# Kernel tuning notes

Measured on AMD Instinct MI355X. Metric: run time of the kernel, lower is better.

Reference implementation:

```python
import jax, jax.numpy as jnp
import numpy as np


def rotary_pos_emb(x):
    # x: [..., seq, dim], dim even. Interleaved (GPT-NeoX-style pairwise) rotary.
    dim, seq = x.shape[-1], x.shape[-2]
    ts = jnp.arange(0, dim, 2, dtype=jnp.float32)
    inv_freqs = 10000.0 ** (-ts / dim)
    grid = jnp.arange(seq, dtype=jnp.float32)[:, None] * inv_freqs[None, :]  # [s, dim//2]
    sin = jnp.repeat(jnp.sin(grid), 2, axis=-1).astype(x.dtype)  # [s, dim]
    cos = jnp.repeat(jnp.cos(grid), 2, axis=-1).astype(x.dtype)  # [s, dim]
    x1, x2 = x[..., ::2], x[..., 1::2]
    xs = jnp.stack([-x2, x1], axis=-1).reshape(x.shape)  # interleave (-x2, x1)
    return x * cos + xs * sin


def setup_inputs() -> dict:
    key = jax.random.key(0)
    kx, kq, kk, kv, ko = jax.random.split(key, 5)
    B, S, D = 2, 2048, 1024
    scale = 1.0 / np.sqrt(D)
    x = jax.random.normal(kx, (B, S, D), dtype=jnp.float32)
    mask = jnp.tril(jnp.ones((S, S), dtype=bool))  # causal
    Wq = jax.random.normal(kq, (D, D), dtype=jnp.float32) * scale
    Wk = jax.random.normal(kk, (D, D), dtype=jnp.float32) * scale
    Wv = jax.random.normal(kv, (D, D), dtype=jnp.float32) * scale
    Wo = jax.random.normal(ko, (D, D), dtype=jnp.float32) * scale
    return {"x": x, "mask": mask, "Wq": Wq, "Wk": Wk, "Wv": Wv, "Wo": Wo}


def reference(x, mask, Wq, Wk, Wv, Wo):
    H = 16
    POS_PORTION = 0.5
    B, S, D = x.shape
    K = D // H
    p = int(K * POS_PORTION)

    q = (x @ Wq) / (K ** 0.5)
    q = q.reshape(B, S, H, K).transpose(0, 2, 1, 3)  # b h l k
    q = jnp.concatenate([rotary_pos_emb(q[..., :p]), q[..., p:]], axis=-1)

    k = (x @ Wk).reshape(B, S, H, K).transpose(0, 2, 1, 3)
    k = jnp.concatenate([rotary_pos_emb(k[..., :p]), k[..., p:]], axis=-1)

    v = (x @ Wv).reshape(B, S, H, K).transpose(0, 2, 1, 3)

    logits = jnp.einsum('bhik,bhjk->bhij', q, k)
    # full-precision masked softmax
    l32 = logits.astype(jnp.float32)
    l32 = jnp.where(mask, l32, -1e30)
    a = jax.nn.softmax(l32, axis=-1).astype(logits.dtype)

    y = jnp.einsum('bhij,bhjv->bhiv', a, v)
    y = y.transpose(0, 2, 1, 3).reshape(B, S, D)  # b l (h v)
    return y @ Wo
```

## Files before the change

### kernel.cpp

```cpp
#include <hip/hip_runtime.h>
#include <cstdint>
#include <cstddef>

typedef __bf16 bf16;
typedef __bf16 bf16x8 __attribute__((ext_vector_type(8)));
typedef float  f32x4  __attribute__((ext_vector_type(4)));
typedef short  s16x4  __attribute__((ext_vector_type(4)));

#define B_  2
#define S_  2048
#define D_  1024
#define H_  16
#define KH  64

__device__ __forceinline__ void gload_lds16(const bf16* gp, bf16* lds_base) {
    __builtin_amdgcn_global_load_lds(
        (const __attribute__((address_space(1))) unsigned int*)gp,
        (__attribute__((address_space(3))) unsigned int*)lds_base,
        16, 0, 0);
}

__global__ __launch_bounds__(256) void prep(
    const float* __restrict__ x, bf16* __restrict__ xb,
    const float* __restrict__ Wq, const float* __restrict__ Wk,
    const float* __restrict__ Wv, const float* __restrict__ Wo,
    bf16* __restrict__ WqkvT, bf16* __restrict__ WoT)
{
    __shared__ bf16 tl[64][72];
    int z = blockIdx.x;
    if (z < 4096) {
        const int i = (z * 256 + threadIdx.x) * 4;
        const float4 v = *(const float4*)(x + i);
        union { int2 w; bf16 e[4]; } u;
        u.e[0] = (bf16)v.x; u.e[1] = (bf16)v.y;
        u.e[2] = (bf16)v.z; u.e[3] = (bf16)v.w;
        *(int2*)(xb + i) = u.w;
        return;
    }
    z -= 4096;
    const int zx = z & 15, zy = (z >> 4) & 15, zw = z >> 8;
    const float* src = (zw == 0) ? Wq : (zw == 1) ? Wk : (zw == 2) ? Wv : Wo;
    bf16* dst = (zw < 3) ? (WqkvT + (size_t)zw * D_ * D_) : WoT;
    const int r0 = zy * 64;
    const int c0 = zx * 64;
    const int t  = threadIdx.x;
    {
        const int r = t >> 2, cs = (t & 3) * 16;
        const float4* p = (const float4*)(src + (size_t)(r0 + r) * D_ + c0 + cs);
        float4 a0 = p[0], a1 = p[1], a2 = p[2], a3 = p[3];
        tl[cs +  0][r] = (bf16)a0.x; tl[cs +  1][r] = (bf16)a0.y;
        tl[cs +  2][r] = (bf16)a0.z; tl[cs +  3][r] = (bf16)a0.w;
        tl[cs +  4][r] = (bf16)a1.x; tl[cs +  5][r] = (bf16)a1.y;
        tl[cs +  6][r] = (bf16)a1.z; tl[cs +  7][r] = (bf16)a1.w;
        tl[cs +  8][r] = (bf16)a2.x; tl[cs +  9][r] = (bf16)a2.y;
        tl[cs + 10][r] = (bf16)a2.z; tl[cs + 11][r] = (bf16)a2.w;
        tl[cs + 12][r] = (bf16)a3.x; tl[cs + 13][r] = (bf16)a3.y;
        tl[cs + 14][r] = (bf16)a3.z; tl[cs + 15][r] = (bf16)a3.w;
    }
    __syncthreads();
    {
        const int c = t >> 2, rs = (t & 3) * 16;
        union { int4 v[2]; bf16 e[16]; } u;
#pragma unroll
        for (int i = 0; i < 16; ++i) u.e[i] = tl[c][rs + i];
        int4* p = (int4*)(dst + (size_t)(c0 + c) * D_ + r0 + rs);
        p[0] = u.v[0]; p[1] = u.v[1];
    }
}

template <int EPI, int BN>
__global__ __launch_bounds__(256, 2) void gemm_bt(
    const bf16* __restrict__ A, const bf16* __restrict__ BT,
    float* __restrict__ C, int N, int Kd,
    bf16* __restrict__ qp, bf16* __restrict__ kp, bf16* __restrict__ vp)
{
    constexpr int NJF = BN / 32;
    __shared__ bf16 As[128 * 64];
    __shared__ bf16 Bs[BN * 64];
    const int tid  = threadIdx.x;
    const int lane = tid & 63;
    const int wave = tid >> 6;
    const int l15  = lane & 15;
    const int quad = lane >> 4;
    const int m0 = blockIdx.y * 128;
    const int n0 = blockIdx.x * BN;
    const int wm = (wave >> 1) * 64;
    const int wn = (wave & 1) * (BN / 2);

    f32x4 acc[4][NJF];
#pragma unroll
    for (int i = 0; i < 4; ++i)
#pragma unroll
        for (int j = 0; j < NJF; ++j) acc[i][j] = f32x4{0.f, 0.f, 0.f, 0.f};

    for (int k0 = 0; k0 < Kd; k0 += 64) {
        __syncthreads();
#pragma unroll
        for (int c = 0; c < 4; ++c) {
            const int base  = wave * 4096 + c * 1024;
            const int flatb = base + lane * 16;
            const int row   = flatb >> 7;
            const int col   = (flatb & 127) >> 1;
            gload_lds16(A + (size_t)(m0 + row) * Kd + k0 + col, As + (base >> 1));
        }
#pragma unroll
        for (int c = 0; c < NJF; ++c) {
            const int base  = wave * (BN * 32) + c * 1024;
            const int flatb = base + lane * 16;
            const int row   = flatb >> 7;
            const int col   = (flatb & 127) >> 1;
            gload_lds16(BT + (size_t)(n0 + row) * Kd + k0 + col, Bs + (base >> 1));
        }
        __syncthreads();
#pragma unroll
        for (int kk = 0; kk < 64; kk += 32) {
            bf16x8 af[4], bfv[NJF];
#pragma unroll
            for (int i = 0; i < 4; ++i)
                af[i] = *(const bf16x8*)&As[(wm + i * 16 + l15) * 64 + kk + quad * 8];
#pragma unroll
            for (int j = 0; j < NJF; ++j)
                bfv[j] = *(const bf16x8*)&Bs[(wn + j * 16 + l15) * 64 + kk + quad * 8];
#pragma unroll
            for (int i = 0; i < 4; ++i)
#pragma unroll
                for (int j = 0; j < NJF; ++j)
                    acc[i][j] = __builtin_amdgcn_mfma_f32_16x16x32_bf16(
                        af[i], bfv[j], acc[i][j], 0, 0, 0);
        }
    }

#pragma unroll
    for (int i = 0; i < 4; ++i)
#pragma unroll
        for (int j = 0; j < NJF; ++j) {
            const int Rb = m0 + wm + i * 16 + quad * 4;
            const int Cc = n0 + wn + j * 16 + l15;
            if (EPI == 0) {
#pragma unroll
                for (int r = 0; r < 4; ++r)
                    C[(size_t)(Rb + r) * N + Cc] = acc[i][j][r];
            } else {
                const int sec = Cc >> 10, cc = Cc & 1023;
                const int h = cc >> 6, kd = cc & 63;
                if (sec == 2) {
                    const int b = Rb >> 11, s0 = Rb & (S_ - 1);
                    union { s16x4 sv; bf16 e[4]; } pv;
#pragma unroll
                    for (int r = 0; r < 4; ++r) pv.e[r] = (bf16)acc[i][j][r];
                    *(s16x4*)&vp[((size_t)(b * H_ + h) * KH + kd) * S_ + s0] = pv.sv;
                } else {
#pragma unroll
                    for (int r = 0; r < 4; ++r) {
                        const int row = Rb + r;
                        const int b = row >> 11, s = row & (S_ - 1);
                        float v = acc[i][j][r];
                        if (sec == 0) {
                            qp[((size_t)(b * H_ + h) * S_ + s) * KH + kd] =
                                (bf16)(v * 0.1803368801111204f);
                        } else {
                            if ((kd >> 4) < 2) {
                                const float partner = __shfl_xor(v, 1);
                                const float inv = __builtin_exp2f(
                                    -(float)(kd >> 1) * (13.28771237954945f / 16.f));
                                const float ang = (float)s * inv;
                                float sn, cn;
                                __sincosf(ang, &sn, &cn);
                                v = (l15 & 1) ? fmaf(partner, sn, v * cn)
                                              : fmaf(-partner, sn, v * cn);
                            }
                            kp[((size_t)(b * H_ + h) * S_ + s) * KH + kd] = (bf16)v;
                        }
                    }
                }
            }
        }
}

__global__ __launch_bounds__(256, 4) void attn(
    const bf16* __restrict__ q, const bf16* __restrict__ k,
    const bf16* __restrict__ vt, bf16* __restrict__ y)
{
    __shared__ bf16 Ks[2][64 * 64];
    __shared__ bf16 VTs[2][64 * 64];

    const int z  = blockIdx.x;
    const int v_ = z & 7;
    const int u_ = (z >> 3) & 31;
    const int w_ = z >> 8;
    const int bh = u_;
    const int qt = (w_ == 0) ? v_ : (w_ == 1) ? (15 - v_)
                 : (w_ == 2) ? (16 + v_) : (31 - v_);
    const int b  = bh >> 4, h = bh & 15;
    const int t    = threadIdx.x;
    const int lane = t & 63, wave = t >> 6;
    const int l15  = lane & 15, quad = lane >> 4;
    const int wrow = qt * 64 + wave * 16;

    const bf16* kbh = k  + (size_t)bh * S_ * KH;
    const bf16* vbh = vt + (size_t)bh * KH * S_;

    const int srow = lane >> 3;
    const int sg   = (lane & 7) ^ srow;

    auto stage = [&](int jt, int bb) {
        const int j0 = jt * 64;
#pragma unroll
        for (int i = 0; i < 2; ++i) {
            const int c = wave * 2 + i;
            gload_lds16(kbh + (size_t)(j0 + c * 8 + srow) * KH + sg * 8,
                        &Ks[bb][c * 8 * 64]);
            gload_lds16(vbh + (size_t)(c * 8 + srow) * S_ + j0 + sg * 8,
                        &VTs[bb][c * 8 * 64]);
        }
    };

    bf16x8 qf[2];
    {
        const bf16* qp = q + ((size_t)bh * S_ + wrow + l15) * KH + quad * 8;
        qf[0] = *(const bf16x8*)qp;
        qf[1] = *(const bf16x8*)(qp + 32);
        const float s = (float)(wrow + l15);
#pragma unroll
        for (int tt = 0; tt < 4; ++tt) {
            const int i = quad * 4 + tt;
            const float inv = exp2f(-(float)i * (13.28771237954945f / 16.f));
            const float ang = s * inv;
            const float sn = sinf(ang), cn = cosf(ang);
            const float x0 = (float)qf[0][2 * tt], x1 = (float)qf[0][2 * tt + 1];
            qf[0][2 * tt]     = (bf16)(x0 * cn - x1 * sn);
            qf[0][2 * tt + 1] = (bf16)(x1 * cn + x0 * sn);
        }
    }

    s16x4 ones4;
#pragma unroll
    for (int i = 0; i < 4; ++i) ones4[i] = (short)0x3F80;

    f32x4 accO[4], lacc;
#pragma unroll
    for (int j = 0; j < 4; ++j) accO[j] = f32x4{0.f, 0.f, 0.f, 0.f};
    lacc = f32x4{0.f, 0.f, 0.f, 0.f};

    const int nj = qt + 1;
    stage(0, 0);
    for (int jt = 0; jt < nj; ++jt) {
        const int bb = jt & 1;
        __syncthreads();
        if (jt + 1 < nj) stage(jt + 1, bb ^ 1);

        f32x4 accS[4];
#pragma unroll
        for (int nb = 0; nb < 4; ++nb) accS[nb] = f32x4{0.f, 0.f, 0.f, 0.f};
#pragma unroll
        for (int c = 0; c < 2; ++c) {
            bf16x8 kf[4];
#pragma unroll
            for (int nb = 0; nb < 4; ++nb)
                kf[nb] = *(const bf16x8*)
                    &Ks[bb][(nb * 16 + l15) * 64 + (((c * 4 + quad) ^ (l15 & 7)) * 8)];
            __builtin_amdgcn_s_setprio(1);
#pragma unroll
            for (int nb = 0; nb < 4; ++nb)
                accS[nb] = __builtin_amdgcn_mfma_f32_16x16x32_bf16(
                    kf[nb], qf[c], accS[nb], 0, 0, 0);
            __builtin_amdgcn_s_setprio(0);
        }

        if (jt == nj - 1) {
            const int j0 = jt * 64;
            const int qi = wrow + l15;
#pragma unroll
            for (int nb = 0; nb < 4; ++nb)
#pragma unroll
                for (int r = 0; r < 4; ++r) {
                    const int ki = j0 + nb * 16 + quad * 4 + r;
                    if (ki > qi) accS[nb][r] = -1e30f;
                }
        }

        s16x4 pf[4];
#pragma unroll
        for (int nb = 0; nb < 4; ++nb) {
            union { bf16 hh[4]; s16x4 ss; } u;
#pragma unroll
            for (int r = 0; r < 4; ++r)
                u.hh[r] = (bf16)__builtin_amdgcn_exp2f(accS[nb][r]);
            pf[nb] = u.ss;
        }

#pragma unroll
        for (int nb = 0; nb < 4; ++nb) {
            s16x4 vf[4];
#pragma unroll
            for (int vb = 0; vb < 4; ++vb)
                vf[vb] = *(const s16x4*)
                    &VTs[bb][(vb * 16 + l15) * 64 +
                             (((nb * 2 + (quad >> 1)) ^ (l15 & 7)) * 8) + (quad & 1) * 4];
            __builtin_amdgcn_s_setprio(1);
#pragma unroll
            for (int vb = 0; vb < 4; ++vb)
                accO[vb] = __builtin_amdgcn_mfma_f32_16x16x16bf16_1k(
                    pf[nb], vf[vb], accO[vb], 0, 0, 0);
            lacc = __builtin_amdgcn_mfma_f32_16x16x16bf16_1k(
                pf[nb], ones4, lacc, 0, 0, 0);
            __builtin_amdgcn_s_setprio(0);
        }
    }

    float rinv[4];
#pragma unroll
    for (int r = 0; r < 4; ++r) rinv[r] = 1.0f / lacc[r];
#pragma unroll
    for (int vb = 0; vb < 4; ++vb)
#pragma unroll
        for (int r = 0; r < 4; ++r) {
            const int row = wrow + quad * 4 + r;
            const int col = h * KH + vb * 16 + l15;
            y[((size_t)b * S_ + row) * D_ + col] = (bf16)(accO[vb][r] * rinv[r]);
        }
}

extern "C" void kernel_launch(void* const* d_in, const int* in_sizes, int n_in,
                              void* d_out, int out_size, void* d_ws, size_t ws_size,
                              hipStream_t stream)
{
    (void)in_sizes; (void)n_in; (void)out_size; (void)ws_size;
    const float* x  = (const float*)d_in[0];
    const float* Wq = (const float*)d_in[2];
    const float* Wk = (const float*)d_in[3];
    const float* Wv = (const float*)d_in[4];
    const float* Wo = (const float*)d_in[5];
    float* out = (float*)d_out;

    char* ws = (char*)d_ws;
    bf16* WqkvT = (bf16*)(ws + 0);
    bf16* WoT   = (bf16*)(ws + 6291456);
    bf16* xb    = (bf16*)(ws + 8388608);
    bf16* qw    = (bf16*)(ws + 16777216);
    bf16* kw    = (bf16*)(ws + 25165824);
    bf16* vtw   = (bf16*)(ws + 33554432);
    bf16* yw    = (bf16*)(ws + 41943040);

    hipLaunchKernelGGL(prep, dim3(5120), dim3(256), 0, stream,
                       x, xb, Wq, Wk, Wv, Wo, WqkvT, WoT);
    hipLaunchKernelGGL((gemm_bt<1, 128>), dim3(24, 32), dim3(256), 0, stream,
                       xb, WqkvT, (float*)nullptr, 3072, 1024, qw, kw, vtw);
    hipLaunchKernelGGL(attn, dim3(1024), dim3(256), 0, stream, qw, kw, vtw, yw);
    hipLaunchKernelGGL((gemm_bt<0, 64>), dim3(16, 32), dim3(256), 0, stream,
                       yw, WoT, out, 1024, 1024,
                       (bf16*)nullptr, (bf16*)nullptr, (bf16*)nullptr);
}
```

Measured before the change: 192.7 us.

## Split attention waves across query and key halves with paired causal tiles

Each attention block now handles two query tiles (p and 31-p) in sequence, which balances causal work per block and halves the grid. Within a tile the four waves form a 2x2 grid: two query halves of 32 rows, each split across two key halves. The partial output and row-sum accumulators are reduced through shared memory before normalisation. This aims to increase MFMA reuse of the K/V fragments loaded from LDS and to balance load across blocks. In exchange it adds extra syncs, an LDS reduction and more registers, with occupancy lowered to 2 blocks per SIMD.

```diff
diff --git a/kernel.cpp b/kernel.cpp
--- a/kernel.cpp
+++ b/kernel.cpp
@@ -177,7 +177,7 @@
         }
 }
 
-__global__ __launch_bounds__(256, 4) void attn(
+__global__ __launch_bounds__(256, 2) void attn(
     const bf16* __restrict__ q, const bf16* __restrict__ k,
     const bf16* __restrict__ vt, bf16* __restrict__ y)
 {
@@ -185,17 +185,14 @@
     __shared__ bf16 VTs[2][64 * 64];
 
     const int z  = blockIdx.x;
-    const int v_ = z & 7;
-    const int u_ = (z >> 3) & 31;
-    const int w_ = z >> 8;
-    const int bh = u_;
-    const int qt = (w_ == 0) ? v_ : (w_ == 1) ? (15 - v_)
-                 : (w_ == 2) ? (16 + v_) : (31 - v_);
+    const int bh = z >> 4;
+    const int p  = z & 15;
     const int b  = bh >> 4, h = bh & 15;
     const int t    = threadIdx.x;
     const int lane = t & 63, wave = t >> 6;
     const int l15  = lane & 15, quad = lane >> 4;
-    const int wrow = qt * 64 + wave * 16;
+    const int wq   = wave >> 1;
+    const int wk   = wave & 1;
 
     const bf16* kbh = k  + (size_t)bh * S_ * KH;
     const bf16* vbh = vt + (size_t)bh * KH * S_;
@@ -215,110 +212,159 @@
         }
     };
 
-    bf16x8 qf[2];
-    {
-        const bf16* qp = q + ((size_t)bh * S_ + wrow + l15) * KH + quad * 8;
-        qf[0] = *(const bf16x8*)qp;
-        qf[1] = *(const bf16x8*)(qp + 32);
-        const float s = (float)(wrow + l15);
-#pragma unroll
-        for (int tt = 0; tt < 4; ++tt) {
-            const int i = quad * 4 + tt;
-            const float inv = exp2f(-(float)i * (13.28771237954945f / 16.f));
-            const float ang = s * inv;
-            const float sn = sinf(ang), cn = cosf(ang);
-            const float x0 = (float)qf[0][2 * tt], x1 = (float)qf[0][2 * tt + 1];
-            qf[0][2 * tt]     = (bf16)(x0 * cn - x1 * sn);
-            qf[0][2 * tt + 1] = (bf16)(x1 * cn + x0 * sn);
-        }
-    }
-
     s16x4 ones4;
 #pragma unroll
     for (int i = 0; i < 4; ++i) ones4[i] = (short)0x3F80;
 
-    f32x4 accO[4], lacc;
-#pragma unroll
-    for (int j = 0; j < 4; ++j) accO[j] = f32x4{0.f, 0.f, 0.f, 0.f};
-    lacc = f32x4{0.f, 0.f, 0.f, 0.f};
-
-    const int nj = qt + 1;
-    stage(0, 0);
-    for (int jt = 0; jt < nj; ++jt) {
-        const int bb = jt & 1;
-        __syncthreads();
-        if (jt + 1 < nj) stage(jt + 1, bb ^ 1);
-
-        f32x4 accS[4];
-#pragma unroll
-        for (int nb = 0; nb < 4; ++nb) accS[nb] = f32x4{0.f, 0.f, 0.f, 0.f};
-#pragma unroll
-        for (int c = 0; c < 2; ++c) {
-            bf16x8 kf[4];
-#pragma unroll
-            for (int nb = 0; nb < 4; ++nb)
-                kf[nb] = *(const bf16x8*)
-                    &Ks[bb][(nb * 16 + l15) * 64 + (((c * 4 + quad) ^ (l15 & 7)) * 8)];
-            __builtin_amdgcn_s_setprio(1);
-#pragma unroll
-            for (int nb = 0; nb < 4; ++nb)
-                accS[nb] = __builtin_amdgcn_mfma_f32_16x16x32_bf16(
-                    kf[nb], qf[c], accS[nb], 0, 0, 0);
-            __builtin_amdgcn_s_setprio(0);
-        }
-
-        if (jt == nj - 1) {
-            const int j0 = jt * 64;
-            const int qi = wrow + l15;
-#pragma unroll
-            for (int nb = 0; nb < 4; ++nb)
-#pragma unroll
-                for (int r = 0; r < 4; ++r) {
-                    const int ki = j0 + nb * 16 + quad * 4 + r;
-                    if (ki > qi) accS[nb][r] = -1e30f;
+    float* red = (wq == 0) ? (float*)&Ks[0][0] : (float*)&VTs[0][0];
+
+    for (int seg = 0; seg < 2; ++seg) {
+        const int qt = seg ? (31 - p) : p;
+        const int q0 = qt * 64 + wq * 32;
+
+        bf16x8 qf[2][2];
+#pragma unroll
+        for (int qb = 0; qb < 2; ++qb) {
+            const bf16* qptr = q + ((size_t)bh * S_ + q0 + qb * 16 + l15) * KH + quad * 8;
+            qf[qb][0] = *(const bf16x8*)qptr;
+            qf[qb][1] = *(const bf16x8*)(qptr + 32);
+            const float s = (float)(q0 + qb * 16 + l15);
+#pragma unroll
+            for (int tt = 0; tt < 4; ++tt) {
+                const int i = quad * 4 + tt;
+                const float inv = exp2f(-(float)i * (13.28771237954945f / 16.f));
+                const float ang = s * inv;
+                const float sn = sinf(ang), cn = cosf(ang);
+                const float x0 = (float)qf[qb][0][2 * tt], x1 = (float)qf[qb][0][2 * tt + 1];
+                qf[qb][0][2 * tt]     = (bf16)(x0 * cn - x1 * sn);
+                qf[qb][0][2 * tt + 1] = (bf16)(x1 * cn + x0 * sn);
+            }
+        }
+
+        f32x4 accO[2][4], lacc[2];
+#pragma unroll
+        for (int qb = 0; qb < 2; ++qb) {
+#pragma unroll
+            for (int vb = 0; vb < 4; ++vb) accO[qb][vb] = f32x4{0.f, 0.f, 0.f, 0.f};
+            lacc[qb] = f32x4{0.f, 0.f, 0.f, 0.f};
+        }
+
+        const int nj = qt + 1;
+        stage(0, 0);
+        for (int jt = 0; jt < nj; ++jt) {
+            const int bb = jt & 1;
+            __syncthreads();
+            if (jt + 1 < nj) stage(jt + 1, bb ^ 1);
+
+            f32x4 accS[2][2];
+#pragma unroll
+            for (int kb = 0; kb < 2; ++kb)
+#pragma unroll
+                for (int qb = 0; qb < 2; ++qb) accS[kb][qb] = f32x4{0.f, 0.f, 0.f, 0.f};
+#pragma unroll
+            for (int c = 0; c < 2; ++c) {
+                bf16x8 kf[2];
+#pragma unroll
+                for (int kb = 0; kb < 2; ++kb)
+                    kf[kb] = *(const bf16x8*)
+                        &Ks[bb][(wk * 32 + kb * 16 + l15) * 64 +
+                                (((c * 4 + quad) ^ (l15 & 7)) * 8)];
+                __builtin_amdgcn_s_setprio(1);
+#pragma unroll
+                for (int kb = 0; kb < 2; ++kb)
+#pragma unroll
+                    for (int qb = 0; qb < 2; ++qb)
+                        accS[kb][qb] = __builtin_amdgcn_mfma_f32_16x16x32_bf16(
+                            kf[kb], qf[qb][c], accS[kb][qb], 0, 0, 0);
+                __builtin_amdgcn_s_setprio(0);
+            }
+
+            if (jt == nj - 1) {
+                const int j0 = jt * 64;
+#pragma unroll
+                for (int kb = 0; kb < 2; ++kb)
+#pragma unroll
+                    for (int qb = 0; qb < 2; ++qb) {
+                        const int qi = q0 + qb * 16 + l15;
+#pragma unroll
+                        for (int r = 0; r < 4; ++r) {
+                            const int ki = j0 + wk * 32 + kb * 16 + quad * 4 + r;
+                            if (ki > qi) accS[kb][qb][r] = -1e30f;
+                        }
+                    }
+            }
+
+            s16x4 pf[2][2];
+#pragma unroll
+            for (int kb = 0; kb < 2; ++kb)
+#pragma unroll
+                for (int qb = 0; qb < 2; ++qb) {
+                    union { bf16 hh[4]; s16x4 ss; } u;
+#pragma unroll
+                    for (int r = 0; r < 4; ++r)
+                        u.hh[r] = (bf16)__builtin_amdgcn_exp2f(accS[kb][qb][r]);
+                    pf[kb][qb] = u.ss;
                 }
-        }
-
-        s16x4 pf[4];
-#pragma unroll
-        for (int nb = 0; nb < 4; ++nb) {
-            union { bf16 hh[4]; s16x4 ss; } u;
-#pragma unroll
-            for (int r = 0; r < 4; ++r)
-                u.hh[r] = (bf16)__builtin_amdgcn_exp2f(accS[nb][r]);
-            pf[nb] = u.ss;
-        }
-
-#pragma unroll
-        for (int nb = 0; nb < 4; ++nb) {
-            s16x4 vf[4];
-#pragma unroll
-            for (int vb = 0; vb < 4; ++vb)
-                vf[vb] = *(const s16x4*)
-                    &VTs[bb][(vb * 16 + l15) * 64 +
-                             (((nb * 2 + (quad >> 1)) ^ (l15 & 7)) * 8) + (quad & 1) * 4];
-            __builtin_amdgcn_s_setprio(1);
-#pragma unroll
-            for (int vb = 0; vb < 4; ++vb)
-                accO[vb] = __builtin_amdgcn_mfma_f32_16x16x16bf16_1k(
-                    pf[nb], vf[vb], accO[vb], 0, 0, 0);
-            lacc = __builtin_amdgcn_mfma_f32_16x16x16bf16_1k(
-                pf[nb], ones4, lacc, 0, 0, 0);
-            __builtin_amdgcn_s_setprio(0);
-        }
-    }
-
-    float rinv[4];
-#pragma unroll
-    for (int r = 0; r < 4; ++r) rinv[r] = 1.0f / lacc[r];
-#pragma unroll
-    for (int vb = 0; vb < 4; ++vb)
-#pragma unroll
-        for (int r = 0; r < 4; ++r) {
-            const int row = wrow + quad * 4 + r;
-            const int col = h * KH + vb * 16 + l15;
-            y[((size_t)b * S_ + row) * D_ + col] = (bf16)(accO[vb][r] * rinv[r]);
-        }
+
+#pragma unroll
+            for (int kb = 0; kb < 2; ++kb) {
+                s16x4 vf[4];
+#pragma unroll
+                for (int vb = 0; vb < 4; ++vb)
+                    vf[vb] = *(const s16x4*)
+                        &VTs[bb][(vb * 16 + l15) * 64 +
+                                 (((wk * 4 + kb * 2 + (quad >> 1)) ^ (l15 & 7)) * 8) +
+                                 (quad & 1) * 4];
+                __builtin_amdgcn_s_setprio(1);
+#pragma unroll
+                for (int qb = 0; qb < 2; ++qb) {
+#pragma unroll
+                    for (int vb = 0; vb < 4; ++vb)
+                        accO[qb][vb] = __builtin_amdgcn_mfma_f32_16x16x16bf16_1k(
+                            pf[kb][qb], vf[vb], accO[qb][vb], 0, 0, 0);
+                    lacc[qb] = __builtin_amdgcn_mfma_f32_16x16x16bf16_1k(
+                        pf[kb][qb], ones4, lacc[qb], 0, 0, 0);
+                }
+                __builtin_amdgcn_s_setprio(0);
+            }
+        }
+
+        __syncthreads();
+        if (wk == 1) {
+#pragma unroll
+            for (int qb = 0; qb < 2; ++qb) {
+#pragma unroll
+                for (int vb = 0; vb < 4; ++vb)
+#pragma unroll
+                    for (int r = 0; r < 4; ++r)
+                        red[(((qb * 4 + vb) * 4) + r) * 64 + lane] = accO[qb][vb][r];
+#pragma unroll
+                for (int r = 0; r < 4; ++r)
+                    red[(32 + qb * 4 + r) * 64 + lane] = lacc[qb][r];
+            }
+        }
+        __syncthreads();
+        if (wk == 0) {
+#pragma unroll
+            for (int qb = 0; qb < 2; ++qb) {
+                float rinv[4];
+#pragma unroll
+                for (int r = 0; r < 4; ++r)
+                    rinv[r] = 1.0f / (lacc[qb][r] + red[(32 + qb * 4 + r) * 64 + lane]);
+#pragma unroll
+                for (int vb = 0; vb < 4; ++vb)
+#pragma unroll
+                    for (int r = 0; r < 4; ++r) {
+                        const float o = accO[qb][vb][r] +
+                                        red[(((qb * 4 + vb) * 4) + r) * 64 + lane];
+                        const int row = q0 + qb * 16 + quad * 4 + r;
+                        const int col = h * KH + vb * 16 + l15;
+                        y[((size_t)b * S_ + row) * D_ + col] = (bf16)(o * rinv[r]);
+                    }
+            }
+        }
+        __syncthreads();
+    }
 }
 
 extern "C" void kernel_launch(void* const* d_in, const int* in_sizes, int n_in,
@@ -346,7 +392,7 @@
                        x, xb, Wq, Wk, Wv, Wo, WqkvT, WoT);
     hipLaunchKernelGGL((gemm_bt<1, 128>), dim3(24, 32), dim3(256), 0, stream,
                        xb, WqkvT, (float*)nullptr, 3072, 1024, qw, kw, vtw);
-    hipLaunchKernelGGL(attn, dim3(1024), dim3(256), 0, stream, qw, kw, vtw, yw);
+    hipLaunchKernelGGL(attn, dim3(512), dim3(256), 0, stream, qw, kw, vtw, yw);
     hipLaunchKernelGGL((gemm_bt<0, 64>), dim3(16, 32), dim3(256), 0, stream,
                        yw, WoT, out, 1024, 1024,
                        (bf16*)nullptr, (bf16*)nullptr, (bf16*)nullptr);
```

New measurement: 198.5 us. +3.0%, slower.
